# Performance work log

Measured on AMD Instinct MI355X. Metric: run time of the kernel, lower is better.

Reference implementation:

```python
import jax, jax.numpy as jnp
import numpy as np

ALPHA_IT = 0.7   # GraphLearner.alpha_it
BETA_IT = 0.5    # GraphLearner.beta_it
B = 4            # hardcoded expand(4, -1, -1) => class_num must be 4
EPS = 1e-12      # F.normalize eps


def _edge_emb(x):
    # x: [B, K, n]; L2-normalize over feature dim K, then Gram matrix over nodes
    xn = x / jnp.clip(jnp.linalg.norm(x, axis=1, keepdims=True), EPS)
    return jnp.einsum('bkn,bkm->bnm', xn, xn)  # [B, n, n]


def _gcn(feat, adj, W, b):
    # feat: [B, K, n], adj: [B, n, n], W: [K, K], b: [B, K]
    n = adj.shape[1]
    adj = jnp.clip(adj, 0.0) + jnp.eye(n, dtype=adj.dtype)[None]
    d = adj.sum(-1)                                   # [B, n]
    dinv = jnp.where(d > 0, d ** -0.5, 0.0)           # inf -> 0 as in torch
    # D A D expressed as row/col scaling (equivalent to the dense diag bmm)
    norm_adj = dinv[:, :, None] * adj * dinv[:, None, :]
    x = feat.transpose(0, 2, 1)                        # [B, n, K]
    pre = x @ W                                        # [B, n, K]
    out = norm_adj @ pre + b[:, None, :]               # [B, n, K]
    return jnp.tanh(out[:, 0, :])                      # [B, K]


def setup_inputs() -> dict:
    key = jax.random.key(0)
    ks = jax.random.split(key, 7)
    C, D = 4, 512
    stdv = 1.0 / np.sqrt(D)
    return {
        'base_text_features': jax.random.normal(ks[0], (C, D), dtype=jnp.float32),
        'base_img_features': jax.random.normal(ks[1], (C, D), dtype=jnp.float32),
        'img_feature': jax.random.normal(ks[2], (40960, D), dtype=jnp.float32),
        'W_tt': jax.random.uniform(ks[3], (D, D), minval=-stdv, maxval=stdv, dtype=jnp.float32),
        'b_tt': jnp.zeros((C, D), dtype=jnp.float32),
        'W_it': jax.random.uniform(ks[4], (D, D), minval=-stdv, maxval=stdv, dtype=jnp.float32),
        'b_it': jnp.zeros((C, D), dtype=jnp.float32),
    }


def reference(base_text_features, base_img_features, img_feature, W_tt, b_tt, W_it, b_it):
    # torch computes feats/edges under no_grad + detach
    bt = jax.lax.stop_gradient(base_text_features)
    bi = jax.lax.stop_gradient(base_img_features)
    D = bt.shape[1]
    inputs_text = bt[:, None, :]                              # [4, 1, D]
    node_tt = jnp.broadcast_to(bt[None], (B, B, D))           # [4, 4, D]
    node_it = jnp.broadcast_to(bi[None], (B, B, D))
    feat_tt = jnp.concatenate([inputs_text, node_tt], axis=1).transpose(0, 2, 1)  # [4, D, 5]
    feat_it = jnp.concatenate([inputs_text, node_it], axis=1).transpose(0, 2, 1)
    edge_tt = _edge_emb(feat_tt)                              # [4, 5, 5]
    edge_it = _edge_emb(feat_it)
    g_tt = _gcn(feat_tt, edge_tt, W_tt, b_tt)                 # [4, D]
    g_it = _gcn(feat_it, edge_it, W_it, b_it)
    graph_o_t = ALPHA_IT * g_tt + (1.0 - ALPHA_IT) * g_it
    refined = BETA_IT * base_text_features + (1.0 - BETA_IT) * graph_o_t
    return (refined, img_feature)
```

## Files before the change

kernel.cpp:

```cpp
#include <hip/hip_runtime.h>

#define DD 512
#define CC 4
#define EPSF 1e-12f

__global__ __launch_bounds__(512) void graph_fused(
    const float* __restrict__ bt,
    const float* __restrict__ bi,
    const float* __restrict__ img,
    const float* __restrict__ Wtt,
    const float* __restrict__ btt,
    const float* __restrict__ Wit,
    const float* __restrict__ bit_,
    float* __restrict__ out)
{
    const int bid = blockIdx.x;
    const int tid = threadIdx.x;

    if (bid >= CC) {
        const float4* __restrict__ src = (const float4*)img;
        float4* __restrict__ dst = (float4*)(out + CC * DD);
        const long long n4 = (40960LL * 512) / 4;
        long long idx = (long long)(bid - CC) * blockDim.x + tid;
        const long long stride = (long long)(gridDim.x - CC) * blockDim.x;
        for (; idx < n4; idx += stride) dst[idx] = src[idx];
        return;
    }

    const int b = bid;
    __shared__ float dots[24];
    __shared__ float coef[9];
    __shared__ float u_tt[DD];
    __shared__ float u_it[DD];

    const int pi_[10] = {0,0,0,0,1,1,1,2,2,3};
    const int pj_[10] = {0,1,2,3,1,2,3,2,3,3};

    const int wave = tid >> 6;
    const int lane = tid & 63;
    for (int dotid = wave; dotid < 24; dotid += 8) {
        const float *u, *v;
        if (dotid < 10)      { u = bt + pi_[dotid] * DD;      v = bt + pj_[dotid] * DD; }
        else if (dotid < 20) { u = bi + pi_[dotid - 10] * DD; v = bi + pj_[dotid - 10] * DD; }
        else                 { u = bt + b * DD;               v = bi + (dotid - 20) * DD; }
        float s = 0.f;
        #pragma unroll
        for (int e = lane; e < DD; e += 64) s += u[e] * v[e];
        #pragma unroll
        for (int off = 32; off; off >>= 1) s += __shfl_xor(s, off, 64);
        if (lane == 0) dots[dotid] = s;
    }
    __syncthreads();

    if (tid == 0) {
        auto pidx = [](int i, int j) -> int {
            if (i > j) { int t = i; i = j; j = t; }
            const int base[4] = {0, 4, 7, 9};
            return base[i] + (j - i);
        };
        float ntn[4], nin[4];
        for (int i = 0; i < 4; i++) ntn[i] = fmaxf(sqrtf(dots[pidx(i, i)]), EPSF);
        for (int i = 0; i < 4; i++) nin[i] = fmaxf(sqrtf(dots[10 + pidx(i, i)]), EPSF);

        {
            int map[5] = {b, 0, 1, 2, 3};
            float adj[5][5];
            for (int r = 0; r < 5; r++)
                for (int c = 0; c < 5; c++) {
                    float cv = dots[pidx(map[r], map[c])] / (ntn[map[r]] * ntn[map[c]]);
                    adj[r][c] = fmaxf(cv, 0.f) + (r == c ? 1.f : 0.f);
                }
            float dinv[5];
            for (int r = 0; r < 5; r++) {
                float dd = 0.f;
                for (int c = 0; c < 5; c++) dd += adj[r][c];
                dinv[r] = 1.0f / sqrtf(dd);
            }
            float w[5];
            for (int j = 0; j < 5; j++) w[j] = dinv[0] * adj[0][j] * dinv[j];
            float ct[4] = {w[1], w[2], w[3], w[4]};
            ct[b] += w[0];
            for (int i = 0; i < 4; i++) coef[i] = ct[i];
        }
        {
            float adj[5][5];
            for (int r = 0; r < 5; r++)
                for (int c = 0; c < 5; c++) {
                    float cv;
                    if (r == 0 && c == 0)      cv = dots[pidx(b, b)] / (ntn[b] * ntn[b]);
                    else if (r == 0)           cv = dots[20 + (c - 1)] / (ntn[b] * nin[c - 1]);
                    else if (c == 0)           cv = dots[20 + (r - 1)] / (ntn[b] * nin[r - 1]);
                    else                       cv = dots[10 + pidx(r - 1, c - 1)] / (nin[r - 1] * nin[c - 1]);
                    adj[r][c] = fmaxf(cv, 0.f) + (r == c ? 1.f : 0.f);
                }
            float dinv[5];
            for (int r = 0; r < 5; r++) {
                float dd = 0.f;
                for (int c = 0; c < 5; c++) dd += adj[r][c];
                dinv[r] = 1.0f / sqrtf(dd);
            }
            float w[5];
            for (int j = 0; j < 5; j++) w[j] = dinv[0] * adj[0][j] * dinv[j];
            coef[4] = w[0];
            for (int j = 0; j < 4; j++) coef[5 + j] = w[j + 1];
        }
    }
    __syncthreads();

    {
        float s1 = 0.f;
        #pragma unroll
        for (int i = 0; i < 4; i++) s1 += coef[i] * bt[i * DD + tid];
        u_tt[tid] = s1;
        float s2 = coef[4] * bt[b * DD + tid];
        #pragma unroll
        for (int j = 0; j < 4; j++) s2 += coef[5 + j] * bi[j * DD + tid];
        u_it[tid] = s2;
    }
    __syncthreads();

    const int d = tid;
    float acc_tt = 0.f, acc_it = 0.f;
    #pragma unroll 8
    for (int k = 0; k < DD; k++) {
        acc_tt += u_tt[k] * Wtt[k * DD + d];
        acc_it += u_it[k] * Wit[k * DD + d];
    }
    const float g_tt = tanhf(acc_tt + btt[b * DD + d]);
    const float g_it = tanhf(acc_it + bit_[b * DD + d]);
    const float go   = 0.7f * g_tt + 0.3f * g_it;
    out[b * DD + d]  = 0.5f * bt[b * DD + d] + 0.5f * go;
}

extern "C" void kernel_launch(void* const* d_in, const int* in_sizes, int n_in,
                              void* d_out, int out_size, void* d_ws, size_t ws_size,
                              hipStream_t stream) {
    const float* bt   = (const float*)d_in[0];
    const float* bi   = (const float*)d_in[1];
    const float* img  = (const float*)d_in[2];
    const float* Wtt  = (const float*)d_in[3];
    const float* btt  = (const float*)d_in[4];
    const float* Wit  = (const float*)d_in[5];
    const float* bit_ = (const float*)d_in[6];
    float* out = (float*)d_out;

    graph_fused<<<2048, 512, 0, stream>>>(bt, bi, img, Wtt, btt, Wit, bit_, out);
}
```

Before: 197.7 us.

## Split GCN matvec across 16 column blocks with k-slice reduction; unroll nontemporal copy

Before, four blocks each handled one class and every thread looped over all 512 rows of both weight matrices. Now 16 blocks each own 32 output columns for all four classes. Each block splits the k dimension into 16 slices, reduces partials through shared memory, and loads every weight once for all four classes. The 84 MB image copy now uses a fixed grid where each thread does 5 unrolled nontemporal vector loads and stores, replacing the strided loop. Each block redundantly recomputes all 36 dot products and coefficients, and the copy relies on the exact size dividing evenly.

New measurement: 163.8 us. 17.2% less time.

```diff
diff --git a/kernel.cpp b/kernel.cpp
--- a/kernel.cpp
+++ b/kernel.cpp
@@ -1,8 +1,13 @@
 #include <hip/hip_runtime.h>
 
 #define DD 512
-#define CC 4
+#define NMM 16
+#define COLS 32
+#define SLICES 16
+#define NCOPY 2048
 #define EPSF 1e-12f
+
+typedef float f32x4 __attribute__((ext_vector_type(4)));
 
 __global__ __launch_bounds__(512) void graph_fused(
     const float* __restrict__ bt,
@@ -17,119 +22,176 @@
     const int bid = blockIdx.x;
     const int tid = threadIdx.x;
 
-    if (bid >= CC) {
-        const float4* __restrict__ src = (const float4*)img;
-        float4* __restrict__ dst = (float4*)(out + CC * DD);
-        const long long n4 = (40960LL * 512) / 4;
-        long long idx = (long long)(bid - CC) * blockDim.x + tid;
-        const long long stride = (long long)(gridDim.x - CC) * blockDim.x;
-        for (; idx < n4; idx += stride) dst[idx] = src[idx];
+    if (bid >= NMM) {
+        const f32x4* __restrict__ src = (const f32x4*)img;
+        f32x4* __restrict__ dst = (f32x4*)(out + 4 * DD);
+        const long long t = (long long)(bid - NMM) * 512 + tid;
+        const long long S = (long long)NCOPY * 512;
+        f32x4 v0 = __builtin_nontemporal_load(&src[t + 0 * S]);
+        f32x4 v1 = __builtin_nontemporal_load(&src[t + 1 * S]);
+        f32x4 v2 = __builtin_nontemporal_load(&src[t + 2 * S]);
+        f32x4 v3 = __builtin_nontemporal_load(&src[t + 3 * S]);
+        f32x4 v4 = __builtin_nontemporal_load(&src[t + 4 * S]);
+        __builtin_nontemporal_store(v0, &dst[t + 0 * S]);
+        __builtin_nontemporal_store(v1, &dst[t + 1 * S]);
+        __builtin_nontemporal_store(v2, &dst[t + 2 * S]);
+        __builtin_nontemporal_store(v3, &dst[t + 3 * S]);
+        __builtin_nontemporal_store(v4, &dst[t + 4 * S]);
         return;
     }
 
-    const int b = bid;
-    __shared__ float dots[24];
-    __shared__ float coef[9];
-    __shared__ float u_tt[DD];
-    __shared__ float u_it[DD];
-
-    const int pi_[10] = {0,0,0,0,1,1,1,2,2,3};
-    const int pj_[10] = {0,1,2,3,1,2,3,2,3,3};
-
-    const int wave = tid >> 6;
-    const int lane = tid & 63;
-    for (int dotid = wave; dotid < 24; dotid += 8) {
-        const float *u, *v;
-        if (dotid < 10)      { u = bt + pi_[dotid] * DD;      v = bt + pj_[dotid] * DD; }
-        else if (dotid < 20) { u = bi + pi_[dotid - 10] * DD; v = bi + pj_[dotid - 10] * DD; }
-        else                 { u = bt + b * DD;               v = bi + (dotid - 20) * DD; }
-        float s = 0.f;
-        #pragma unroll
-        for (int e = lane; e < DD; e += 64) s += u[e] * v[e];
-        #pragma unroll
-        for (int off = 32; off; off >>= 1) s += __shfl_xor(s, off, 64);
-        if (lane == 0) dots[dotid] = s;
-    }
-    __syncthreads();
-
-    if (tid == 0) {
+    __shared__ float dots[36];
+    __shared__ float coef[4][9];
+    __shared__ float u[2][4][DD];
+    __shared__ float red[8][SLICES][COLS];
+
+    {
+        const int pi_[10] = {0,0,0,0,1,1,1,2,2,3};
+        const int pj_[10] = {0,1,2,3,1,2,3,2,3,3};
+        const int wave = tid >> 6;
+        const int lane = tid & 63;
+        for (int dotid = wave; dotid < 36; dotid += 8) {
+            const float *uu, *vv;
+            if (dotid < 10)      { uu = bt + pi_[dotid] * DD;      vv = bt + pj_[dotid] * DD; }
+            else if (dotid < 20) { uu = bi + pi_[dotid - 10] * DD; vv = bi + pj_[dotid - 10] * DD; }
+            else { int r = dotid - 20; uu = bt + (r >> 2) * DD;    vv = bi + (r & 3) * DD; }
+            float s = 0.f;
+            #pragma unroll
+            for (int e = lane; e < DD; e += 64) s += uu[e] * vv[e];
+            #pragma unroll
+            for (int off = 32; off; off >>= 1) s += __shfl_xor(s, off, 64);
+            if (lane == 0) dots[dotid] = s;
+        }
+    }
+    __syncthreads();
+
+    if (tid < 4) {
+        const int b = tid;
         auto pidx = [](int i, int j) -> int {
             if (i > j) { int t = i; i = j; j = t; }
             const int base[4] = {0, 4, 7, 9};
             return base[i] + (j - i);
         };
         float ntn[4], nin[4];
+        #pragma unroll
         for (int i = 0; i < 4; i++) ntn[i] = fmaxf(sqrtf(dots[pidx(i, i)]), EPSF);
+        #pragma unroll
         for (int i = 0; i < 4; i++) nin[i] = fmaxf(sqrtf(dots[10 + pidx(i, i)]), EPSF);
 
         {
             int map[5] = {b, 0, 1, 2, 3};
             float adj[5][5];
+            #pragma unroll
             for (int r = 0; r < 5; r++)
+                #pragma unroll
                 for (int c = 0; c < 5; c++) {
                     float cv = dots[pidx(map[r], map[c])] / (ntn[map[r]] * ntn[map[c]]);
                     adj[r][c] = fmaxf(cv, 0.f) + (r == c ? 1.f : 0.f);
                 }
             float dinv[5];
+            #pragma unroll
             for (int r = 0; r < 5; r++) {
                 float dd = 0.f;
+                #pragma unroll
                 for (int c = 0; c < 5; c++) dd += adj[r][c];
                 dinv[r] = 1.0f / sqrtf(dd);
             }
             float w[5];
+            #pragma unroll
             for (int j = 0; j < 5; j++) w[j] = dinv[0] * adj[0][j] * dinv[j];
             float ct[4] = {w[1], w[2], w[3], w[4]};
             ct[b] += w[0];
-            for (int i = 0; i < 4; i++) coef[i] = ct[i];
+            #pragma unroll
+            for (int i = 0; i < 4; i++) coef[b][i] = ct[i];
         }
         {
             float adj[5][5];
+            #pragma unroll
             for (int r = 0; r < 5; r++)
+                #pragma unroll
                 for (int c = 0; c < 5; c++) {
                     float cv;
                     if (r == 0 && c == 0)      cv = dots[pidx(b, b)] / (ntn[b] * ntn[b]);
-                    else if (r == 0)           cv = dots[20 + (c - 1)] / (ntn[b] * nin[c - 1]);
-                    else if (c == 0)           cv = dots[20 + (r - 1)] / (ntn[b] * nin[r - 1]);
+                    else if (r == 0)           cv = dots[20 + b * 4 + (c - 1)] / (ntn[b] * nin[c - 1]);
+                    else if (c == 0)           cv = dots[20 + b * 4 + (r - 1)] / (ntn[b] * nin[r - 1]);
                     else                       cv = dots[10 + pidx(r - 1, c - 1)] / (nin[r - 1] * nin[c - 1]);
                     adj[r][c] = fmaxf(cv, 0.f) + (r == c ? 1.f : 0.f);
                 }
             float dinv[5];
+            #pragma unroll
             for (int r = 0; r < 5; r++) {
                 float dd = 0.f;
+                #pragma unroll
                 for (int c = 0; c < 5; c++) dd += adj[r][c];
                 dinv[r] = 1.0f / sqrtf(dd);
             }
             float w[5];
+            #pragma unroll
             for (int j = 0; j < 5; j++) w[j] = dinv[0] * adj[0][j] * dinv[j];
-            coef[4] = w[0];
-            for (int j = 0; j < 4; j++) coef[5 + j] = w[j + 1];
+            coef[b][4] = w[0];
+            #pragma unroll
+            for (int j = 0; j < 4; j++) coef[b][5 + j] = w[j + 1];
         }
     }
     __syncthreads();
 
     {
-        float s1 = 0.f;
-        #pragma unroll
-        for (int i = 0; i < 4; i++) s1 += coef[i] * bt[i * DD + tid];
-        u_tt[tid] = s1;
-        float s2 = coef[4] * bt[b * DD + tid];
-        #pragma unroll
-        for (int j = 0; j < 4; j++) s2 += coef[5 + j] * bi[j * DD + tid];
-        u_it[tid] = s2;
-    }
-    __syncthreads();
-
-    const int d = tid;
-    float acc_tt = 0.f, acc_it = 0.f;
-    #pragma unroll 8
-    for (int k = 0; k < DD; k++) {
-        acc_tt += u_tt[k] * Wtt[k * DD + d];
-        acc_it += u_it[k] * Wit[k * DD + d];
-    }
-    const float g_tt = tanhf(acc_tt + btt[b * DD + d]);
-    const float g_it = tanhf(acc_it + bit_[b * DD + d]);
-    const float go   = 0.7f * g_tt + 0.3f * g_it;
-    out[b * DD + d]  = 0.5f * bt[b * DD + d] + 0.5f * go;
+        const int k = tid;
+        #pragma unroll
+        for (int b = 0; b < 4; b++) {
+            float s1 = 0.f;
+            #pragma unroll
+            for (int i = 0; i < 4; i++) s1 += coef[b][i] * bt[i * DD + k];
+            u[0][b][k] = s1;
+            float s2 = coef[b][4] * bt[b * DD + k];
+            #pragma unroll
+            for (int j = 0; j < 4; j++) s2 += coef[b][5 + j] * bi[j * DD + k];
+            u[1][b][k] = s2;
+        }
+    }
+    __syncthreads();
+
+    {
+        const int c  = tid & (COLS - 1);
+        const int ks = tid >> 5;
+        const int col = bid * COLS + c;
+        const int k0 = ks * (DD / SLICES);
+        float acc[2][4] = {};
+        const float* __restrict__ Ws[2] = {Wtt, Wit};
+        #pragma unroll
+        for (int m = 0; m < 2; m++) {
+            const float* __restrict__ W = Ws[m];
+            #pragma unroll 8
+            for (int kk = 0; kk < DD / SLICES; kk++) {
+                const int k = k0 + kk;
+                const float w = W[k * DD + col];
+                #pragma unroll
+                for (int b = 0; b < 4; b++) acc[m][b] += u[m][b][k] * w;
+            }
+        }
+        #pragma unroll
+        for (int m = 0; m < 2; m++)
+            #pragma unroll
+            for (int b = 0; b < 4; b++)
+                red[m * 4 + b][ks][c] = acc[m][b];
+    }
+    __syncthreads();
+
+    if (tid < 4 * COLS) {
+        const int c = tid & (COLS - 1);
+        const int b = tid >> 5;
+        const int col = bid * COLS + c;
+        float stt = 0.f, sit = 0.f;
+        #pragma unroll
+        for (int s = 0; s < SLICES; s++) {
+            stt += red[b][s][c];
+            sit += red[4 + b][s][c];
+        }
+        const float g_tt = tanhf(stt + btt[b * DD + col]);
+        const float g_it = tanhf(sit + bit_[b * DD + col]);
+        const float go   = 0.7f * g_tt + 0.3f * g_it;
+        out[b * DD + col] = 0.5f * bt[b * DD + col] + 0.5f * go;
+    }
 }
 
 extern "C" void kernel_launch(void* const* d_in, const int* in_sizes, int n_in,
@@ -144,5 +206,5 @@
     const float* bit_ = (const float*)d_in[6];
     float* out = (float*)d_out;
 
-    graph_fused<<<2048, 512, 0, stream>>>(bt, bi, img, Wtt, btt, Wit, bit_, out);
+    graph_fused<<<NMM + NCOPY, 512, 0, stream>>>(bt, bi, img, Wtt, btt, Wit, bit_, out);
 }
```
